# Performance work log

Hardware: AMD Instinct MI355X
Metric: run time of the kernel (lower is better)

## Reference

```python
import jax, jax.numpy as jnp
import numpy as np

B, T = 256, 50
N_ITEMS = 100000
EMB = 256      # embedding
KBD = 128      # KBembedding == MN_dims
HID = 256      # layers[0] == layers[-1]
OUT = 256      # out_dim
NF = 10        # MN_nfactors == n_r


def setup_inputs() -> dict:
    key = jax.random.key(0)
    ks = jax.random.split(key, 18)
    s = 0.05
    return {
        "X": jax.random.randint(ks[0], (B, T), 0, N_ITEMS),
        "E": jax.random.normal(ks[1], (N_ITEMS, EMB), jnp.float32) * s,
        "KBE": jax.random.normal(ks[2], (N_ITEMS, KBD), jnp.float32) * s,
        "r_matrix": jax.random.normal(ks[3], (NF, KBD), jnp.float32) * s,
        "W_ih": jax.random.normal(ks[4], (3 * HID, EMB), jnp.float32) * s,
        "W_hh": jax.random.normal(ks[5], (3 * HID, HID), jnp.float32) * s,
        "b_ih": jnp.zeros((3 * HID,), jnp.float32),
        "b_hh": jnp.zeros((3 * HID,), jnp.float32),
        "MNu_W": jax.random.normal(ks[6], (KBD, HID), jnp.float32) * s,
        "MNu_b": jnp.zeros((KBD,), jnp.float32),
        "MNu2_W": jax.random.normal(ks[7], (HID, KBD + HID), jnp.float32) * s,
        "MNu2_b": jnp.zeros((HID,), jnp.float32),
        "MNea_W": jax.random.normal(ks[8], (KBD, KBD), jnp.float32) * s,
        "MNea_b": jnp.zeros((KBD,), jnp.float32),
        "mlp1_W": jax.random.normal(ks[9], (OUT, HID), jnp.float32) * s,
        "mlp1_b": jnp.zeros((OUT,), jnp.float32),
        "mlp2_W": jax.random.normal(ks[10], (OUT, EMB + KBD), jnp.float32) * s,
        "mlp2_b": jnp.zeros((OUT,), jnp.float32),
    }


def _gru_cell(x, h, W_ih, W_hh, b_ih, b_hh):
    # PyTorch GRUCell: gates stacked [r, z, n] along dim 0 of weights
    gi = x @ W_ih.T + b_ih
    gh = h @ W_hh.T + b_hh
    ir, iz, inn = jnp.split(gi, 3, axis=-1)
    hr, hz, hn = jnp.split(gh, 3, axis=-1)
    r = jax.nn.sigmoid(ir + hr)
    z = jax.nn.sigmoid(iz + hz)
    n = jnp.tanh(inn + r * hn)
    return (1.0 - z) * n + z * h


def reference(X, E, KBE, r_matrix, W_ih, W_hh, b_ih, b_hh,
              MNu_W, MNu_b, MNu2_W, MNu2_b, MNea_W, MNea_b,
              mlp1_W, mlp1_b, mlp2_W, mlp2_b):
    Bv, Tv = X.shape
    Em = E.at[0].set(0.0)     # mask row 0 of E
    KBm = KBE.at[0].set(0.0)  # mask row 0 of KBE
    Sx = Em[X]                # (B, T, EMB)
    KBItem = KBm[X]           # (B, T, KBD)

    def step(carry, xs):
        h, MN, y_sum = carry
        x_t, kb_t = xs                      # (B, EMB), (B, KBD)
        h = _gru_cell(x_t, h, W_ih, W_hh, b_ih, b_hh)
        y = h                                # dropout p=0 -> identity
        # gated memory write
        EA = jnp.tanh(kb_t @ MNea_W.T + MNea_b)          # (B, KBD)
        EA = EA[:, None, :] + r_matrix                    # (B, NF, KBD)
        gate = jax.nn.sigmoid(jnp.sum(MN * EA, axis=-1, keepdims=True))  # (B, NF, 1)
        MN = MN * (1.0 - gate) + EA * gate
        # attention read
        U = jnp.tanh(y @ MNu_W.T + MNu_b)                 # (B, KBD)
        AW = jax.nn.softmax(U @ r_matrix.T, axis=1)       # (B, NF)
        AC = jnp.einsum('bfd,bf->bd', MN, AW)             # (B, KBD)
        Ut = jnp.tanh(jnp.concatenate([y, AC], axis=-1) @ MNu2_W.T + MNu2_b)  # (B, HID)
        y_out = jnp.tanh(Ut @ mlp1_W.T + mlp1_b)          # (B, OUT)
        return (h, MN, y_sum + y_out), None

    init = (jnp.zeros((Bv, HID), Sx.dtype),
            jnp.zeros((Bv, NF, KBD), Sx.dtype),
            jnp.zeros((Bv, OUT), Sx.dtype))
    xs = (jnp.swapaxes(Sx, 0, 1), jnp.swapaxes(KBItem, 0, 1))  # (T, B, *)
    (h, MN, y_sum), _ = jax.lax.scan(step, init, xs)
    y = y_sum / Tv

    MergeE = jnp.concatenate([E, KBE], axis=1).at[0].set(0.0)  # (N, EMB+KBD)
    Sy = jnp.tanh(MergeE @ mlp2_W.T + mlp2_b)                  # (N, OUT)
    scores = jax.nn.log_softmax(y @ Sy.T, axis=1)              # (B, N)
    return scores, y
```

## Files before the change

### kernel.cpp

```cpp
#include <hip/hip_runtime.h>

typedef _Float16 f16;
typedef _Float16 f16x8 __attribute__((ext_vector_type(8)));
typedef float f32x4 __attribute__((ext_vector_type(4)));

#define MFMA16(a,b,c) __builtin_amdgcn_mfma_f32_16x16x32_f16(a,b,c,0,0,0)

#define NITEMS 100000
#define NBLK4  1563

#define OFF_WIH   0u
#define OFF_WHH   393216u
#define OFF_MNU   786432u
#define OFF_MNU2  851968u
#define OFF_MNEA  1048576u
#define OFF_MLP1  1081344u
#define OFF_MLP2  1212416u
#define OFF_GI    1409024u
#define OFF_TV    21069824u
#define OFF_MN    24346624u
#define OFF_YALL  57114624u
#define OFF_SY    66945024u
#define OFF_Y16   118407168u
#define OFF_PMAX  118538240u
#define OFF_PSUM  120176640u
#define OFF_LSE   121815040u

__device__ __forceinline__ float sigm(float x) { return 1.f / (1.f + __expf(-x)); }
__device__ __forceinline__ float tanh_fast(float x) {
  return 1.f - 2.f / (1.f + __expf(2.f * x));
}

__global__ __launch_bounds__(256) void k_pack(
    const float* s0, const float* s1, const float* s2, const float* s3,
    const float* s4, const float* s5, const float* s6, f16* base)
{
  int fid = blockIdx.x * 256 + threadIdx.x;
  const float* src; f16* dst; int K, f;
  if (fid < 24576)      { src = s0; dst = base;          K = 256; f = fid; }
  else if (fid < 49152) { src = s1; dst = base + 196608; K = 256; f = fid - 24576; }
  else if (fid < 53248) { src = s2; dst = base + 393216; K = 256; f = fid - 49152; }
  else if (fid < 65536) { src = s3; dst = base + 425984; K = 384; f = fid - 53248; }
  else if (fid < 67584) { src = s4; dst = base + 524288; K = 128; f = fid - 65536; }
  else if (fid < 75776) { src = s5; dst = base + 540672; K = 256; f = fid - 67584; }
  else                  { src = s6; dst = base + 606208; K = 384; f = fid - 75776; }
  int lane = f & 63, t2 = f >> 6, KS = K >> 5;
  int ks = t2 % KS, nt = t2 / KS;
  int row = nt * 16 + (lane & 15), col = ks * 32 + ((lane >> 4) << 3);
  const float* sp = src + (size_t)row * K + col;
  f16x8 v;
  #pragma unroll
  for (int j = 0; j < 8; j++) v[j] = (f16)sp[j];
  *(f16x8*)(dst + (size_t)f * 8) = v;
}

__global__ __launch_bounds__(512) void k_giea(
    const int* __restrict__ X, const float* __restrict__ E,
    const f16* __restrict__ Wih_p, const float* __restrict__ bih, f16* __restrict__ gi,
    const float* __restrict__ KBE, const f16* __restrict__ Wea_p,
    const float* __restrict__ bea, f16* __restrict__ tv)
{
  __shared__ __align__(16) f16 At[32][264];
  int tid = threadIdx.x;
  int w = tid >> 6, lane = tid & 63, lr = lane & 15, lg = lane >> 4;
  if (blockIdx.x < 400) {
    int r0 = blockIdx.x * 32;
    int t = r0 >> 8;
    {
      int r = tid >> 4, c = (tid & 15) * 16;
      int b = (r0 + r) & 255;
      int item = X[b * 50 + t];
      if (item == 0) {
        #pragma unroll
        for (int j = 0; j < 16; j++) At[r][c + j] = (f16)0.f;
      } else {
        const float4* sp = (const float4*)(E + (size_t)item * 256 + c);
        #pragma unroll
        for (int q = 0; q < 4; q++) {
          float4 v = sp[q];
          At[r][c + q*4 + 0] = (f16)v.x; At[r][c + q*4 + 1] = (f16)v.y;
          At[r][c + q*4 + 2] = (f16)v.z; At[r][c + q*4 + 3] = (f16)v.w;
        }
      }
    }
    __syncthreads();
    f32x4 acc[2][6] = {};
    for (int ks = 0; ks < 8; ks++) {
      f16x8 a0 = *(const f16x8*)(&At[lr][ks * 32 + lg * 8]);
      f16x8 a1 = *(const f16x8*)(&At[16 + lr][ks * 32 + lg * 8]);
      #pragma unroll
      for (int j = 0; j < 6; j++) {
        int nt = w * 6 + j;
        f16x8 bf = *(const f16x8*)(Wih_p + ((size_t)((nt * 8 + ks) * 64 + lane) << 3));
        acc[0][j] = MFMA16(a0, bf, acc[0][j]);
        acc[1][j] = MFMA16(a1, bf, acc[1][j]);
      }
    }
    #pragma unroll
    for (int j = 0; j < 6; j++) {
      int col = (w * 6 + j) * 16 + lr;
      float bias = bih[col];
      #pragma unroll
      for (int mt = 0; mt < 2; mt++)
        #pragma unroll
        for (int rr = 0; rr < 4; rr++) {
          int row = r0 + mt * 16 + lg * 4 + rr;
          gi[(size_t)row * 768 + col] = (f16)(acc[mt][j][rr] + bias);
        }
    }
  } else {
    int r0 = (blockIdx.x - 400) * 32;
    int t = r0 >> 8;
    {
      int r = tid >> 4, c = (tid & 15) * 8;
      int b = (r0 + r) & 255;
      int item = X[b * 50 + t];
      if (item == 0) {
        #pragma unroll
        for (int j = 0; j < 8; j++) At[r][c + j] = (f16)0.f;
      } else {
        const float4* sp = (const float4*)(KBE + (size_t)item * 128 + c);
        #pragma unroll
        for (int q = 0; q < 2; q++) {
          float4 v = sp[q];
          At[r][c + q*4 + 0] = (f16)v.x; At[r][c + q*4 + 1] = (f16)v.y;
          At[r][c + q*4 + 2] = (f16)v.z; At[r][c + q*4 + 3] = (f16)v.w;
        }
      }
    }
    __syncthreads();
    f32x4 acc[2] = {};
    for (int ks = 0; ks < 4; ks++) {
      f16x8 a0 = *(const f16x8*)(&At[lr][ks * 32 + lg * 8]);
      f16x8 a1 = *(const f16x8*)(&At[16 + lr][ks * 32 + lg * 8]);
      f16x8 bf = *(const f16x8*)(Wea_p + ((size_t)((w * 4 + ks) * 64 + lane) << 3));
      acc[0] = MFMA16(a0, bf, acc[0]);
      acc[1] = MFMA16(a1, bf, acc[1]);
    }
    int col = w * 16 + lr;
    float bias = bea[col];
    #pragma unroll
    for (int mt = 0; mt < 2; mt++)
      #pragma unroll
      for (int rr = 0; rr < 4; rr++) {
        int row = r0 + mt * 16 + lg * 4 + rr;
        tv[(size_t)row * 128 + col] = (f16)tanh_fast(acc[mt][rr] + bias);
      }
  }
}

__global__ __launch_bounds__(1024)
__attribute__((amdgpu_waves_per_eu(4, 4)))
void k_fused(
    const f16* __restrict__ Whh_p, const float* __restrict__ bhh,
    const f16* __restrict__ gi, f16* __restrict__ y_all,
    const f16* __restrict__ tv, const float* __restrict__ Rm, f16* __restrict__ MN,
    const float* __restrict__ E, const float* __restrict__ KBE,
    const f16* __restrict__ mlp2_p, const float* __restrict__ mlp2b, f16* __restrict__ Sy)
{
  __shared__ __align__(16) char smem[147456];
  int tid = threadIdx.x, w = tid >> 6, lane = tid & 63, lr = lane & 15, lg = lane >> 4;

  if (blockIdx.x < 32) {
    f16* Wlds = (f16*)smem;
    f16* hb0 = (f16*)(smem + 131072);
    f16* hb1 = (f16*)(smem + 139264);
    int r0 = blockIdx.x * 8;
    {
      const float4* src = (const float4*)Whh_p;
      float4* dst = (float4*)Wlds;
      #pragma unroll
      for (int i = 0; i < 8; i++) dst[tid + i * 1024] = src[tid + i * 1024];
      float4 z4 = {0.f, 0.f, 0.f, 0.f};
      ((float4*)hb0)[tid] = z4;
    }
    int col = w * 16 + lr;
    float bR = bhh[col], bZ = bhh[col + 256], bN = bhh[col + 512];
    float hreg[4] = {0.f, 0.f, 0.f, 0.f};
    const f16* gP = gi + (size_t)(r0 + lg * 4) * 768 + col;
    f16 P[4][3];
    if (lg < 2) {
      #pragma unroll
      for (int rr = 0; rr < 4; rr++)
        #pragma unroll
        for (int g = 0; g < 3; g++)
          P[rr][g] = gP[rr * 768 + g * 256];
    }
    __syncthreads();
    f16* hc = hb0; f16* hn_ = hb1;
    int xr = (lr & 7) << 4;
    const f16* wB0 = Wlds + (size_t)w * 4096 + lane * 8;
    const f16* wBz = Whh_p + ((size_t)((16 + w) * 8) * 64 + lane) * 8;
    const f16* wBn = Whh_p + ((size_t)((32 + w) * 8) * 64 + lane) * 8;
    for (int t = 0; t < 50; t++) {
      f32x4 aR = {}, aZ = {}, aN = {};
      const char* hbase = (const char*)hc + lr * 512;
      #pragma unroll
      for (int ks = 0; ks < 8; ks++) {
        f16x8 a = *(const f16x8*)(hbase + ((ks * 64 + lg * 16) ^ xr));
        aR = MFMA16(a, *(const f16x8*)(wB0 + ks * 512), aR);
        aZ = MFMA16(a, *(const f16x8*)(wBz + ks * 512), aZ);
        aN = MFMA16(a, *(const f16x8*)(wBn + ks * 512), aN);
      }
      if (lg < 2) {
        #pragma unroll
        for (int rr = 0; rr < 4; rr++) {
          int row = lg * 4 + rr;
          float rg = sigm((float)P[rr][0] + aR[rr] + bR);
          float zg = sigm((float)P[rr][1] + aZ[rr] + bZ);
          float ng = tanh_fast((float)P[rr][2] + rg * (aN[rr] + bN));
          float hv = ng + zg * (hreg[rr] - ng);
          hreg[rr] = hv;
          *(f16*)((char*)hn_ + row * 512 + ((col * 2) ^ ((row & 7) << 4))) = (f16)hv;
        }
        if (t < 49) {
          const f16* gN = gP + (size_t)(t + 1) * 196608;
          #pragma unroll
          for (int rr = 0; rr < 4; rr++)
            #pragma unroll
            for (int g = 0; g < 3; g++)
              P[rr][g] = gN[rr * 768 + g * 256];
        }
      }
      __syncthreads();
      if (tid < 256) {
        int row = tid >> 5, c = tid & 31;
        f16x8 hv = *(const f16x8*)((char*)hn_ + row * 512 + ((c * 16) ^ ((row & 7) << 4)));
        *(f16x8*)(y_all + ((size_t)t * 256 + r0 + row) * 256 + c * 8) = hv;
      }
      f16* tmp = hc; hc = hn_; hn_ = tmp;
    }
  } else if (blockIdx.x < 192) {
    int pair = (blockIdx.x - 32) * 16 + w;
    int b = pair / 10, f = pair - (pair / 10) * 10;
    float r0_ = Rm[f * 128 + lane], r1_ = Rm[f * 128 + 64 + lane];
    float mn0 = 0.f, mn1 = 0.f;
    float c0 = (float)tv[(size_t)b * 128 + lane];
    float c1 = (float)tv[(size_t)b * 128 + 64 + lane];
    for (int t = 0; t < 50; t++) {
      float ea0 = c0 + r0_;
      float ea1 = c1 + r1_;
      if (t < 49) {
        size_t nb = ((size_t)(t + 1) * 256 + b) * 128;
        c0 = (float)tv[nb + lane];
        c1 = (float)tv[nb + 64 + lane];
      }
      float p = mn0 * ea0 + mn1 * ea1;
      #pragma unroll
      for (int off = 32; off > 0; off >>= 1) p += __shfl_xor(p, off);
      float g = sigm(p);
      mn0 += (ea0 - mn0) * g;
      mn1 += (ea1 - mn1) * g;
      size_t mb = (((size_t)t * 256 + b) * 10 + f) * 128;
      MN[mb + lane] = (f16)mn0;
      MN[mb + 64 + lane] = (f16)mn1;
    }
  } else {
    f16* At = (f16*)smem;
    int i0 = (blockIdx.x - 192) * 32;
    {
      int r = tid >> 5;
      int item = i0 + r;
      int c = (tid & 31) * 8;
      if (item == 0) {
        #pragma unroll
        for (int j = 0; j < 8; j++) At[r * 392 + c + j] = (f16)0.f;
      } else {
        const float4* sp = (const float4*)(E + (size_t)item * 256 + c);
        #pragma unroll
        for (int q = 0; q < 2; q++) {
          float4 v = sp[q];
          At[r * 392 + c + q*4 + 0] = (f16)v.x; At[r * 392 + c + q*4 + 1] = (f16)v.y;
          At[r * 392 + c + q*4 + 2] = (f16)v.z; At[r * 392 + c + q*4 + 3] = (f16)v.w;
        }
      }
      int c2 = (tid & 31) * 4;
      if (item == 0) {
        #pragma unroll
        for (int j = 0; j < 4; j++) At[r * 392 + 256 + c2 + j] = (f16)0.f;
      } else {
        float4 v = *(const float4*)(KBE + (size_t)item * 128 + c2);
        At[r * 392 + 256 + c2 + 0] = (f16)v.x; At[r * 392 + 256 + c2 + 1] = (f16)v.y;
        At[r * 392 + 256 + c2 + 2] = (f16)v.z; At[r * 392 + 256 + c2 + 3] = (f16)v.w;
      }
    }
    __syncthreads();
    int mt = w & 1, ntp = w >> 1;
    f32x4 acc[2] = {};
    for (int ks = 0; ks < 12; ks++) {
      f16x8 a = *(const f16x8*)(&At[(mt * 16 + lr) * 392 + ks * 32 + lg * 8]);
      #pragma unroll
      for (int j = 0; j < 2; j++) {
        int nt = ntp * 2 + j;
        f16x8 bf = *(const f16x8*)(mlp2_p + ((size_t)((nt * 12 + ks) * 64 + lane) << 3));
        acc[j] = MFMA16(a, bf, acc[j]);
      }
    }
    #pragma unroll
    for (int j = 0; j < 2; j++) {
      int col = (ntp * 2 + j) * 16 + lr;
      float bias = mlp2b[col];
      #pragma unroll
      for (int rr = 0; rr < 4; rr++) {
        int item = i0 + mt * 16 + lg * 4 + rr;
        Sy[(size_t)item * 256 + col] = (f16)tanh_fast(acc[j][rr] + bias);
      }
    }
  }
}

__global__ __launch_bounds__(512) void k_uacut(
    const f16* __restrict__ y_all, const f16* __restrict__ MNu_p,
    const float* __restrict__ MNub, const float* __restrict__ Rm,
    const f16* __restrict__ MN,
    const f16* __restrict__ MNu2_p, const float* __restrict__ MNu2b,
    const f16* __restrict__ mlp1_p, const float* __restrict__ mlp1b,
    float* __restrict__ ypart)
{
  __shared__ __align__(16) char smem[25088];
  int tid = threadIdx.x, w = tid >> 6, lane = tid & 63, lr = lane & 15, lg = lane >> 4;
  f16   (*Aty)[264] = (f16(*)[264])smem;
  float (*Uf)[136]  = (float(*)[136])(smem + 8448);
  f16   (*Utl)[264] = (f16(*)[264])(smem + 8448);
  float (*Lg)[10]   = (float(*)[10])(smem + 17152);
  float (*Aw)[10]   = (float(*)[10])(smem + 17792);
  f16   (*ACs)[136] = (f16(*)[136])(smem + 18432);
  int r0 = blockIdx.x * 16;
  {
    int r = tid >> 5, c = (tid & 31) * 8;
    f16x8 v = *(const f16x8*)(y_all + (size_t)(r0 + r) * 256 + c);
    *(f16x8*)(&Aty[r][c]) = v;
  }
  __syncthreads();
  {
    f32x4 acc = {};
    for (int ks = 0; ks < 8; ks++) {
      f16x8 a = *(const f16x8*)(&Aty[lr][ks * 32 + lg * 8]);
      f16x8 bf = *(const f16x8*)(MNu_p + ((size_t)((w * 8 + ks) * 64 + lane) << 3));
      acc = MFMA16(a, bf, acc);
    }
    int col = w * 16 + lr;
    float bias = MNub[col];
    #pragma unroll
    for (int rr = 0; rr < 4; rr++)
      Uf[lg * 4 + rr][col] = tanh_fast(acc[rr] + bias);
  }
  __syncthreads();
  if (tid < 160) {
    int row = tid / 10, f = tid - (tid / 10) * 10;
    float s = 0.f;
    for (int d = 0; d < 128; d++) s += Uf[row][d] * Rm[f * 128 + d];
    Lg[row][f] = s;
  }
  __syncthreads();
  if (tid < 16) {
    float m = -1e30f;
    #pragma unroll
    for (int f = 0; f < 10; f++) m = fmaxf(m, Lg[tid][f]);
    float e[10], s = 0.f;
    #pragma unroll
    for (int f = 0; f < 10; f++) { e[f] = __expf(Lg[tid][f] - m); s += e[f]; }
    float inv = 1.f / s;
    #pragma unroll
    for (int f = 0; f < 10; f++) Aw[tid][f] = e[f] * inv;
  }
  __syncthreads();
  if (tid < 256) {
    int row = tid >> 4, d0 = (tid & 15) * 8;
    float a[8] = {0,0,0,0,0,0,0,0};
    for (int f = 0; f < 10; f++) {
      float wgt = Aw[row][f];
      f16x8 mv = *(const f16x8*)(MN + (((size_t)(r0 + row)) * 10 + f) * 128 + d0);
      #pragma unroll
      for (int q = 0; q < 8; q++) a[q] += wgt * (float)mv[q];
    }
    f16x8 o;
    #pragma unroll
    for (int q = 0; q < 8; q++) o[q] = (f16)a[q];
    *(f16x8*)(&ACs[row][d0]) = o;
  }
  __syncthreads();
  {
    f32x4 acc[2] = {};
    for (int ks = 0; ks < 12; ks++) {
      f16x8 a = (ks < 8)
        ? *(const f16x8*)(&Aty[lr][ks * 32 + lg * 8])
        : *(const f16x8*)(&ACs[lr][(ks - 8) * 32 + lg * 8]);
      #pragma unroll
      for (int j = 0; j < 2; j++) {
        f16x8 bf = *(const f16x8*)(MNu2_p + ((size_t)(((w * 2 + j) * 12 + ks) * 64 + lane) << 3));
        acc[j] = MFMA16(a, bf, acc[j]);
      }
    }
    __syncthreads();
    #pragma unroll
    for (int j = 0; j < 2; j++) {
      int col = (w * 2 + j) * 16 + lr;
      float bias = MNu2b[col];
      #pragma unroll
      for (int rr = 0; rr < 4; rr++)
        Utl[lg * 4 + rr][col] = (f16)tanh_fast(acc[j][rr] + bias);
    }
  }
  __syncthreads();
  {
    f32x4 acc2[2] = {};
    for (int ks = 0; ks < 8; ks++) {
      f16x8 a = *(const f16x8*)(&Utl[lr][ks * 32 + lg * 8]);
      #pragma unroll
      for (int j = 0; j < 2; j++) {
        f16x8 bf = *(const f16x8*)(mlp1_p + ((size_t)(((w * 2 + j) * 8 + ks) * 64 + lane) << 3));
        acc2[j] = MFMA16(a, bf, acc2[j]);
      }
    }
    #pragma unroll
    for (int j = 0; j < 2; j++) {
      int col = (w * 2 + j) * 16 + lr;
      float bias = mlp1b[col];
      #pragma unroll
      for (int rr = 0; rr < 4; rr++) {
        int row = r0 + lg * 4 + rr;
        ypart[(size_t)row * 256 + col] = tanh_fast(acc2[j][rr] + bias);
      }
    }
  }
}

__global__ __launch_bounds__(256) void k_yfin(
    const float* __restrict__ ypart, float* __restrict__ outy, f16* __restrict__ y16)
{
  int b = blockIdx.x, c = threadIdx.x;
  float s = 0.f;
  for (int t = 0; t < 50; t++) s += ypart[((size_t)t * 256 + b) * 256 + c];
  float v = s * (1.0f / 50.0f);
  outy[b * 256 + c] = v;
  y16[b * 256 + c] = (f16)v;
}

__global__ __launch_bounds__(512) void k_score0(
    const f16* __restrict__ y16, const f16* __restrict__ Sy,
    float* __restrict__ pmax, float* __restrict__ psum)
{
  __shared__ float pm[512], ps[512];
  int tid = threadIdx.x, w = tid >> 6, lane = tid & 63, lr = lane & 15, lg = lane >> 4;
  int i0 = blockIdx.x * 64;
  int mtb = (w >> 1) * 4, ntb = (w & 1) * 2;
  f32x4 acc[4][2] = {};
  for (int ks = 0; ks < 8; ks++) {
    f16x8 a[4];
    #pragma unroll
    for (int i = 0; i < 4; i++)
      a[i] = *(const f16x8*)(y16 + ((size_t)((mtb + i) * 16 + lr)) * 256 + ks * 32 + lg * 8);
    #pragma unroll
    for (int j = 0; j < 2; j++) {
      int item = i0 + (ntb + j) * 16 + lr;
      int ic = item < NITEMS ? item : (NITEMS - 1);
      f16x8 bv = *(const f16x8*)(Sy + (size_t)ic * 256 + ks * 32 + lg * 8);
      #pragma unroll
      for (int i = 0; i < 4; i++) acc[i][j] = MFMA16(a[i], bv, acc[i][j]);
    }
  }
  {
    int item0 = i0 + ntb * 16 + lr, item1 = item0 + 16;
    bool v0 = item0 < NITEMS, v1 = item1 < NITEMS;
    #pragma unroll
    for (int i = 0; i < 4; i++)
      #pragma unroll
      for (int rr = 0; rr < 4; rr++) {
        float x0 = v0 ? acc[i][0][rr] : -1e30f;
        float x1 = v1 ? acc[i][1][rr] : -1e30f;
        float m = fmaxf(x0, x1);
        m = fmaxf(m, __shfl_xor(m, 1)); m = fmaxf(m, __shfl_xor(m, 2));
        m = fmaxf(m, __shfl_xor(m, 4)); m = fmaxf(m, __shfl_xor(m, 8));
        float s = (v0 ? __expf(x0 - m) : 0.f) + (v1 ? __expf(x1 - m) : 0.f);
        s += __shfl_xor(s, 1); s += __shfl_xor(s, 2);
        s += __shfl_xor(s, 4); s += __shfl_xor(s, 8);
        if (lr == 0) {
          int row = (mtb + i) * 16 + lg * 4 + rr;
          pm[(w & 1) * 256 + row] = m;
          ps[(w & 1) * 256 + row] = s;
        }
      }
  }
  __syncthreads();
  if (tid < 256) {
    float m0 = pm[tid], m1 = pm[256 + tid];
    float s0 = ps[tid], s1 = ps[256 + tid];
    float M = fmaxf(m0, m1);
    float S = s0 * __expf(m0 - M) + s1 * __expf(m1 - M);
    pmax[(size_t)tid * 1600 + blockIdx.x] = M;
    psum[(size_t)tid * 1600 + blockIdx.x] = S;
  }
}

__global__ __launch_bounds__(256) void k_lse(
    const float* __restrict__ pmax, const float* __restrict__ psum, float* __restrict__ lse)
{
  int b = blockIdx.x, tid = threadIdx.x;
  __shared__ float red[256];
  float m = -1e30f;
  for (int i = tid; i < NBLK4; i += 256) m = fmaxf(m, pmax[(size_t)b * 1600 + i]);
  red[tid] = m; __syncthreads();
  for (int s = 128; s > 0; s >>= 1) {
    if (tid < s) red[tid] = fmaxf(red[tid], red[tid + s]);
    __syncthreads();
  }
  float M = red[0]; __syncthreads();
  float s = 0.f;
  for (int i = tid; i < NBLK4; i += 256)
    s += psum[(size_t)b * 1600 + i] * __expf(pmax[(size_t)b * 1600 + i] - M);
  red[tid] = s; __syncthreads();
  for (int q = 128; q > 0; q >>= 1) {
    if (tid < q) red[tid] += red[tid + q];
    __syncthreads();
  }
  if (tid == 0) lse[b] = M + logf(red[0]);
}

__global__ __launch_bounds__(512) void k_scores1(
    const f16* __restrict__ y16, const f16* __restrict__ Sy,
    const float* __restrict__ lse, float* __restrict__ out)
{
  __shared__ float lse_s[256];
  int tid = threadIdx.x, w = tid >> 6, lane = tid & 63, lr = lane & 15, lg = lane >> 4;
  if (tid < 256) lse_s[tid] = lse[tid];
  int i0 = blockIdx.x * 64;
  int mtb = (w >> 1) * 4, ntb = (w & 1) * 2;
  f32x4 acc[4][2] = {};
  for (int ks = 0; ks < 8; ks++) {
    f16x8 a[4];
    #pragma unroll
    for (int i = 0; i < 4; i++)
      a[i] = *(const f16x8*)(y16 + ((size_t)((mtb + i) * 16 + lr)) * 256 + ks * 32 + lg * 8);
    #pragma unroll
    for (int j = 0; j < 2; j++) {
      int item = i0 + (ntb + j) * 16 + lr;
      int ic = item < NITEMS ? item : (NITEMS - 1);
      f16x8 bv = *(const f16x8*)(Sy + (size_t)ic * 256 + ks * 32 + lg * 8);
      #pragma unroll
      for (int i = 0; i < 4; i++) acc[i][j] = MFMA16(a[i], bv, acc[i][j]);
    }
  }
  __syncthreads();
  #pragma unroll
  for (int i = 0; i < 4; i++)
    #pragma unroll
    for (int j = 0; j < 2; j++) {
      int c = i0 + (ntb + j) * 16 + lr;
      if (c < NITEMS) {
        #pragma unroll
        for (int rr = 0; rr < 4; rr++) {
          int row = (mtb + i) * 16 + lg * 4 + rr;
          out[(size_t)row * NITEMS + c] = acc[i][j][rr] - lse_s[row];
        }
      }
    }
}

extern "C" void kernel_launch(void* const* d_in, const int* in_sizes, int n_in,
                              void* d_out, int out_size, void* d_ws, size_t ws_size,
                              hipStream_t stream) {
  (void)in_sizes; (void)n_in; (void)out_size; (void)ws_size;
  const int*   X     = (const int*)d_in[0];
  const float* E     = (const float*)d_in[1];
  const float* KBE   = (const float*)d_in[2];
  const float* Rm    = (const float*)d_in[3];
  const float* Wih   = (const float*)d_in[4];
  const float* Whh   = (const float*)d_in[5];
  const float* bih   = (const float*)d_in[6];
  const float* bhh   = (const float*)d_in[7];
  const float* MNuW  = (const float*)d_in[8];
  const float* MNub  = (const float*)d_in[9];
  const float* MNu2W = (const float*)d_in[10];
  const float* MNu2b = (const float*)d_in[11];
  const float* MNeaW = (const float*)d_in[12];
  const float* MNeab = (const float*)d_in[13];
  const float* mlp1W = (const float*)d_in[14];
  const float* mlp1b = (const float*)d_in[15];
  const float* mlp2W = (const float*)d_in[16];
  const float* mlp2b = (const float*)d_in[17];

  char* ws = (char*)d_ws;
  f16*   Wih_p  = (f16*)(ws + OFF_WIH);
  f16*   Whh_p  = (f16*)(ws + OFF_WHH);
  f16*   MNu_p  = (f16*)(ws + OFF_MNU);
  f16*   MNu2_p = (f16*)(ws + OFF_MNU2);
  f16*   Wea_p  = (f16*)(ws + OFF_MNEA);
  f16*   mlp1_p = (f16*)(ws + OFF_MLP1);
  f16*   mlp2_p = (f16*)(ws + OFF_MLP2);
  f16*   gi     = (f16*)(ws + OFF_GI);
  f16*   tv     = (f16*)(ws + OFF_TV);
  f16*   MN     = (f16*)(ws + OFF_MN);
  f16*   y_all  = (f16*)(ws + OFF_YALL);
  f16*   Sy     = (f16*)(ws + OFF_SY);
  float* ypart  = (float*)(ws + OFF_GI);
  f16*   y16    = (f16*)(ws + OFF_Y16);
  float* pmax   = (float*)(ws + OFF_PMAX);
  float* psum   = (float*)(ws + OFF_PSUM);
  float* lse    = (float*)(ws + OFF_LSE);
  float* outf   = (float*)d_out;

  k_pack<<<344, 256, 0, stream>>>(Wih, Whh, MNuW, MNu2W, MNeaW, mlp1W, mlp2W, (f16*)ws);
  k_giea<<<800, 512, 0, stream>>>(X, E, Wih_p, bih, gi, KBE, Wea_p, MNeab, tv);
  k_fused<<<3317, 1024, 0, stream>>>(Whh_p, bhh, gi, y_all, tv, Rm, MN,
                                     E, KBE, mlp2_p, mlp2b, Sy);
  k_uacut<<<800, 512, 0, stream>>>(y_all, MNu_p, MNub, Rm, MN,
                                   MNu2_p, MNu2b, mlp1_p, mlp1b, ypart);
  k_yfin<<<256, 256, 0, stream>>>(ypart, outf + 25600000, y16);
  k_score0<<<NBLK4, 512, 0, stream>>>(y16, Sy, pmax, psum);
  k_lse<<<256, 256, 0, stream>>>(pmax, psum, lse);
  k_scores1<<<NBLK4, 512, 0, stream>>>(y16, Sy, lse, outf);
}
```

Baseline: 374.8 us.

## Store GRU input gates in per-lane packed layout, fold hidden biases

```diff
diff --git a/kernel.cpp b/kernel.cpp
--- a/kernel.cpp
+++ b/kernel.cpp
@@ -1,6 +1,7 @@
 #include <hip/hip_runtime.h>
 
 typedef _Float16 f16;
+typedef _Float16 f16x4 __attribute__((ext_vector_type(4)));
 typedef _Float16 f16x8 __attribute__((ext_vector_type(8)));
 typedef float f32x4 __attribute__((ext_vector_type(4)));
 
@@ -56,19 +57,23 @@
 
 __global__ __launch_bounds__(512) void k_giea(
     const int* __restrict__ X, const float* __restrict__ E,
-    const f16* __restrict__ Wih_p, const float* __restrict__ bih, f16* __restrict__ gi,
+    const f16* __restrict__ Wih_p, const float* __restrict__ bih,
+    const float* __restrict__ bhh, f16* __restrict__ gi2,
     const float* __restrict__ KBE, const f16* __restrict__ Wea_p,
     const float* __restrict__ bea, f16* __restrict__ tv)
 {
-  __shared__ __align__(16) f16 At[32][264];
+  __shared__ __align__(16) char smem[66048];
+  f16 (*At)[264] = (f16(*)[264])smem;
+  f16* Lg2 = (f16*)(smem + 16896);
   int tid = threadIdx.x;
   int w = tid >> 6, lane = tid & 63, lr = lane & 15, lg = lane >> 4;
   if (blockIdx.x < 400) {
-    int r0 = blockIdx.x * 32;
-    int t = r0 >> 8;
+    int r0g = blockIdx.x * 32;
+    int t = r0g >> 8;
+    int grp0 = (r0g & 255) >> 3;
     {
       int r = tid >> 4, c = (tid & 15) * 16;
-      int b = (r0 + r) & 255;
+      int b = (r0g + r) & 255;
       int item = X[b * 50 + t];
       if (item == 0) {
         #pragma unroll
@@ -96,17 +101,28 @@
         acc[1][j] = MFMA16(a1, bf, acc[1][j]);
       }
     }
+    int lane_s = ((lg & 1) << 4) | lr;
     #pragma unroll
     for (int j = 0; j < 6; j++) {
-      int col = (w * 6 + j) * 16 + lr;
-      float bias = bih[col];
-      #pragma unroll
-      for (int mt = 0; mt < 2; mt++)
-        #pragma unroll
-        for (int rr = 0; rr < 4; rr++) {
-          int row = r0 + mt * 16 + lg * 4 + rr;
-          gi[(size_t)row * 768 + col] = (f16)(acc[mt][j][rr] + bias);
-        }
+      int tile = w * 6 + j;
+      int gate = tile >> 4, w_s = tile & 15;
+      int col = tile * 16 + lr;
+      float bias = bih[col] + (col < 512 ? bhh[col] : 0.f);
+      #pragma unroll
+      for (int mt = 0; mt < 2; mt++) {
+        int grp_local = mt * 2 + (lg >> 1);
+        f16* dstp = Lg2 + (((grp_local * 16 + w_s) * 32 + lane_s) * 12 + gate * 4);
+        #pragma unroll
+        for (int rr = 0; rr < 4; rr++)
+          dstp[rr] = (f16)(acc[mt][j][rr] + bias);
+      }
+    }
+    __syncthreads();
+    f16* dst = gi2 + ((size_t)t * 32 + grp0) * 6144;
+    #pragma unroll
+    for (int q = 0; q < 6; q++) {
+      int i = q * 512 + tid;
+      *(f16x8*)(dst + i * 8) = *(const f16x8*)(Lg2 + i * 8);
     }
   } else {
     int r0 = (blockIdx.x - 400) * 32;
@@ -137,15 +153,19 @@
       acc[0] = MFMA16(a0, bf, acc[0]);
       acc[1] = MFMA16(a1, bf, acc[1]);
     }
+    f16* tvs = Lg2;
     int col = w * 16 + lr;
     float bias = bea[col];
     #pragma unroll
     for (int mt = 0; mt < 2; mt++)
       #pragma unroll
-      for (int rr = 0; rr < 4; rr++) {
-        int row = r0 + mt * 16 + lg * 4 + rr;
-        tv[(size_t)row * 128 + col] = (f16)tanh_fast(acc[mt][rr] + bias);
-      }
+      for (int rr = 0; rr < 4; rr++)
+        tvs[(mt * 16 + lg * 4 + rr) * 128 + col] = (f16)tanh_fast(acc[mt][rr] + bias);
+    __syncthreads();
+    {
+      int row = tid >> 4, c = (tid & 15) * 8;
+      *(f16x8*)(tv + (size_t)(r0 + row) * 128 + c) = *(const f16x8*)(tvs + row * 128 + c);
+    }
   }
 }
 
@@ -153,7 +173,7 @@
 __attribute__((amdgpu_waves_per_eu(4, 4)))
 void k_fused(
     const f16* __restrict__ Whh_p, const float* __restrict__ bhh,
-    const f16* __restrict__ gi, f16* __restrict__ y_all,
+    const f16* __restrict__ gi2, f16* __restrict__ y_all,
     const f16* __restrict__ tv, const float* __restrict__ Rm, f16* __restrict__ MN,
     const float* __restrict__ E, const float* __restrict__ KBE,
     const f16* __restrict__ mlp2_p, const float* __restrict__ mlp2b, f16* __restrict__ Sy)
@@ -175,16 +195,14 @@
       ((float4*)hb0)[tid] = z4;
     }
     int col = w * 16 + lr;
-    float bR = bhh[col], bZ = bhh[col + 256], bN = bhh[col + 512];
+    float bN = bhh[col + 512];
     float hreg[4] = {0.f, 0.f, 0.f, 0.f};
-    const f16* gP = gi + (size_t)(r0 + lg * 4) * 768 + col;
-    f16 P[4][3];
+    const f16* gP = gi2 + (size_t)blockIdx.x * 6144 + (size_t)(w * 32 + lane) * 12;
+    f16x8 P0 = {};
+    f16x4 P1 = {};
     if (lg < 2) {
-      #pragma unroll
-      for (int rr = 0; rr < 4; rr++)
-        #pragma unroll
-        for (int g = 0; g < 3; g++)
-          P[rr][g] = gP[rr * 768 + g * 256];
+      P0 = *(const f16x8*)gP;
+      P1 = *(const f16x4*)(gP + 8);
     }
     __syncthreads();
     f16* hc = hb0; f16* hn_ = hb1;
@@ -206,20 +224,17 @@
         #pragma unroll
         for (int rr = 0; rr < 4; rr++) {
           int row = lg * 4 + rr;
-          float rg = sigm((float)P[rr][0] + aR[rr] + bR);
-          float zg = sigm((float)P[rr][1] + aZ[rr] + bZ);
-          float ng = tanh_fast((float)P[rr][2] + rg * (aN[rr] + bN));
+          float rg = sigm((float)P0[rr] + aR[rr]);
+          float zg = sigm((float)P0[4 + rr] + aZ[rr]);
+          float ng = tanh_fast((float)P1[rr] + rg * (aN[rr] + bN));
           float hv = ng + zg * (hreg[rr] - ng);
           hreg[rr] = hv;
           *(f16*)((char*)hn_ + row * 512 + ((col * 2) ^ ((row & 7) << 4))) = (f16)hv;
         }
         if (t < 49) {
           const f16* gN = gP + (size_t)(t + 1) * 196608;
-          #pragma unroll
-          for (int rr = 0; rr < 4; rr++)
-            #pragma unroll
-            for (int g = 0; g < 3; g++)
-              P[rr][g] = gN[rr * 768 + g * 256];
+          P0 = *(const f16x8*)gN;
+          P1 = *(const f16x4*)(gN + 8);
         }
       }
       __syncthreads();
@@ -588,7 +603,7 @@
   f16*   Wea_p  = (f16*)(ws + OFF_MNEA);
   f16*   mlp1_p = (f16*)(ws + OFF_MLP1);
   f16*   mlp2_p = (f16*)(ws + OFF_MLP2);
-  f16*   gi     = (f16*)(ws + OFF_GI);
+  f16*   gi2    = (f16*)(ws + OFF_GI);
   f16*   tv     = (f16*)(ws + OFF_TV);
   f16*   MN     = (f16*)(ws + OFF_MN);
   f16*   y_all  = (f16*)(ws + OFF_YALL);
@@ -601,8 +616,8 @@
   float* outf   = (float*)d_out;
 
   k_pack<<<344, 256, 0, stream>>>(Wih, Whh, MNuW, MNu2W, MNeaW, mlp1W, mlp2W, (f16*)ws);
-  k_giea<<<800, 512, 0, stream>>>(X, E, Wih_p, bih, gi, KBE, Wea_p, MNeab, tv);
-  k_fused<<<3317, 1024, 0, stream>>>(Whh_p, bhh, gi, y_all, tv, Rm, MN,
+  k_giea<<<800, 512, 0, stream>>>(X, E, Wih_p, bih, bhh, gi2, KBE, Wea_p, MNeab, tv);
+  k_fused<<<3317, 1024, 0, stream>>>(Whh_p, bhh, gi2, y_all, tv, Rm, MN,
                                      E, KBE, mlp2_p, mlp2b, Sy);
   k_uacut<<<800, 512, 0, stream>>>(y_all, MNu_p, MNub, Rm, MN,
                                    MNu2_p, MNu2b, mlp1_p, mlp1b, ypart);
```

New measurement: 368.4 us. No clear change (-1.7%).
